# Kernel tuning notes

Hardware: AMD Instinct MI355X
Metric: run time of the kernel (lower is better)

## Reference

```python
import jax, jax.numpy as jnp
import numpy as np

N_NODES = 100000
N_EDGES = 3200000
N_FEAT = 512
N_CLASS = 10
HIDDEN = 16
EPS = 1e-12  # matches torch F.normalize clamp


def setup_inputs() -> dict:
    key = jax.random.key(0)
    ks = jax.random.split(key, 6)
    x = jax.random.normal(ks[0], (N_NODES, N_FEAT), dtype=jnp.float32)
    edge_index = jax.random.randint(ks[1], (2, N_EDGES), 0, N_NODES, dtype=jnp.int64)
    W1 = jax.random.normal(ks[2], (N_FEAT, HIDDEN), dtype=jnp.float32) / np.sqrt(N_FEAT)
    b1 = jnp.zeros((HIDDEN,), dtype=jnp.float32)
    beta = jnp.ones((1,), dtype=jnp.float32)  # learnable scalar of prop2
    W2 = jax.random.normal(ks[3], (HIDDEN, N_CLASS), dtype=jnp.float32) / np.sqrt(HIDDEN)
    b2 = jnp.zeros((N_CLASS,), dtype=jnp.float32)
    return {"x": x, "edge_index": edge_index, "W1": W1, "b1": b1,
            "beta": beta, "W2": W2, "b2": b2}


def _agnn_conv(h, src, dst, beta_val, n_nodes):
    # L2-normalize node features (cosine attention)
    norm = jnp.maximum(jnp.linalg.norm(h, axis=-1, keepdims=True), EPS)
    hn = h / norm
    # per-edge attention logit: beta * cos(h_i, h_j)
    alpha = beta_val * jnp.sum(hn[src] * hn[dst], axis=-1)  # [E]
    # scatter-softmax over edges sharing the same destination node
    amax = jax.ops.segment_max(alpha, dst, num_segments=n_nodes)
    ea = jnp.exp(alpha - amax[dst])
    denom = jax.ops.segment_sum(ea, dst, num_segments=n_nodes)
    w = ea / denom[dst]  # self-loops guarantee denom > 0
    # weighted aggregation of source features into destination nodes
    return jax.ops.segment_sum(w[:, None] * h[src], dst, num_segments=n_nodes)


def reference(x, edge_index, W1, b1, beta, W2, b2):
    n = x.shape[0]
    # dropout is identity in eval mode
    h = jax.nn.relu(x @ W1 + b1)  # [N, 16]
    # AGNNConv adds self-loops before propagation
    loops = jnp.arange(n, dtype=edge_index.dtype)
    src = jnp.concatenate([edge_index[0], loops])
    dst = jnp.concatenate([edge_index[1], loops])
    h = _agnn_conv(h, src, dst, jnp.float32(1.0), n)   # prop1: beta fixed to 1
    h = _agnn_conv(h, src, dst, beta[0], n)            # prop2: learnable beta
    logits = h @ W2 + b2
    return jax.nn.log_softmax(logits, axis=-1)
```

## Files before the change

kernel.cpp:

```cpp
#include <hip/hip_runtime.h>
#include <hip/hip_fp16.h>
#include <math.h>

#define N_NODES 100000
#define N_EDGES 3200000
#define EPRIME  (N_EDGES + N_NODES)
#define NFEAT   512
#define HID     16
#define NCLS    10

#define NPB     256
#define NB      ((N_NODES + NPB - 1) / NPB)
#define CHUNK   4096
#define NCH     ((EPRIME + CHUNK - 1) / CHUNK)
#define CAPB    10240
#define GBLK    2048

union U2 { unsigned int u; __half2 h; };
__device__ __forceinline__ float2 u2f(unsigned int v) {
  U2 t; t.u = v; return __half22float2(t.h);
}

__global__ __launch_bounds__(256, 4) void k_gemm_norm(const float* __restrict__ x,
                                                      const float* __restrict__ W1,
                                                      const float* __restrict__ b1,
                                                      __half* __restrict__ hn1,
                                                      float* __restrict__ norms1,
                                                      int* __restrict__ gcur) {
  if (blockIdx.x == 0)
    for (int i = threadIdx.x; i < NB; i += 256) gcur[i] = 0;

  __shared__ float red[2][2][2][16];

  const int lane = threadIdx.x & 63;
  const int wv   = threadIdx.x >> 6;
  const int r    = wv >> 1;
  const int h    = wv & 1;
  const int stride = GBLK * 2;
  const int row0 = blockIdx.x * 2 + r;
  const int nIter = (N_NODES - 1 - blockIdx.x * 2) / stride + 1;

  float4 w[4][4];
#pragma unroll
  for (int kk = 0; kk < 4; ++kk)
#pragma unroll
    for (int j = 0; j < 4; ++j)
      w[kk][j] = *reinterpret_cast<const float4*>(
          W1 + (size_t)(h * 256 + lane * 4 + kk) * 16 + j * 4);

  const float bias = (lane < 16) ? b1[lane] : 0.f;
  const int koff = h * 256 + lane * 4;

  const float4 z4 = make_float4(0.f, 0.f, 0.f, 0.f);
  float4 c0 = z4, p0 = z4, t0 = z4;

  if (row0 < N_NODES)
    c0 = *reinterpret_cast<const float4*>(x + (size_t)row0 * NFEAT + koff);
  if (row0 + stride < N_NODES)
    p0 = *reinterpret_cast<const float4*>(x + (size_t)(row0 + stride) * NFEAT + koff);

  for (int i = 0; i < nIter; ++i) {
    const int row = row0 + i * stride;
    const int r2 = row + 2 * stride;
    if (r2 < N_NODES)
      t0 = *reinterpret_cast<const float4*>(x + (size_t)r2 * NFEAT + koff);

    const float xs[4] = {c0.x, c0.y, c0.z, c0.w};

    float acc[16];
#pragma unroll
    for (int j = 0; j < 16; ++j) acc[j] = 0.f;

#pragma unroll
    for (int kk = 0; kk < 4; ++kk) {
      const float xv = xs[kk];
#pragma unroll
      for (int j4 = 0; j4 < 4; ++j4) {
        acc[j4 * 4 + 0] = fmaf(xv, w[kk][j4].x, acc[j4 * 4 + 0]);
        acc[j4 * 4 + 1] = fmaf(xv, w[kk][j4].y, acc[j4 * 4 + 1]);
        acc[j4 * 4 + 2] = fmaf(xv, w[kk][j4].z, acc[j4 * 4 + 2]);
        acc[j4 * 4 + 3] = fmaf(xv, w[kk][j4].w, acc[j4 * 4 + 3]);
      }
    }

#pragma unroll
    for (int j = 0; j < 8; ++j) {
      float send = (lane & 32) ? acc[j] : acc[j + 8];
      float rr = __shfl_xor(send, 32);
      acc[j] = ((lane & 32) ? acc[j + 8] : acc[j]) + rr;
    }
#pragma unroll
    for (int j = 0; j < 4; ++j) {
      float send = (lane & 16) ? acc[j] : acc[j + 4];
      float rr = __shfl_xor(send, 16);
      acc[j] = ((lane & 16) ? acc[j + 4] : acc[j]) + rr;
    }
#pragma unroll
    for (int j = 0; j < 2; ++j) {
      float send = (lane & 8) ? acc[j] : acc[j + 2];
      float rr = __shfl_xor(send, 8);
      acc[j] = ((lane & 8) ? acc[j + 2] : acc[j]) + rr;
    }
    {
      float send = (lane & 4) ? acc[0] : acc[1];
      float rr = __shfl_xor(send, 4);
      acc[0] = ((lane & 4) ? acc[1] : acc[0]) + rr;
    }
    acc[0] += __shfl_xor(acc[0], 2);
    acc[0] += __shfl_xor(acc[0], 1);

    if ((lane & 3) == 0) red[i & 1][r][h][lane >> 2] = acc[0];
    __syncthreads();

    if (h == 0 && row < N_NODES) {
      float v = 0.f;
      if (lane < 16)
        v = fmaxf(red[i & 1][r][0][lane] + red[i & 1][r][1][lane] + bias, 0.f);
      float ss = v * v;
      ss += __shfl_xor(ss, 1);
      ss += __shfl_xor(ss, 2);
      ss += __shfl_xor(ss, 4);
      ss += __shfl_xor(ss, 8);
      const float nrm = sqrtf(ss);
      const float inv = 1.0f / fmaxf(nrm, 1e-12f);
      if (lane < 16) hn1[(size_t)row * HID + lane] = __float2half_rn(v * inv);
      if (lane == 0) norms1[row] = nrm;
    }

    c0 = p0; p0 = t0;
  }
}

__global__ __launch_bounds__(256) void k_part(const int* __restrict__ ei,
                                              int* __restrict__ gcur,
                                              unsigned int* __restrict__ slots) {
  __shared__ int sh_hist[NB];
  __shared__ int sh_gbase[NB];
  const int tid = threadIdx.x;

  for (int i = tid; i < NB; i += 256) sh_hist[i] = 0;
  __syncthreads();

  const int base = blockIdx.x * CHUNK;
  unsigned int pk[16];
  int bk[16], rk[16];
#pragma unroll
  for (int j = 0; j < 16; ++j) {
    int e = base + j * 256 + tid;
    bool valid = (e < EPRIME);
    int srcv = 0, d = 0;
    if (valid) {
      if (e < N_EDGES) { srcv = ei[e]; d = ei[N_EDGES + e]; }
      else             { srcv = d = e - N_EDGES; }
    }
    bk[j] = valid ? (d >> 8) : -1;
    pk[j] = (unsigned)srcv | ((unsigned)(d & 255) << 20);
    rk[j] = valid ? atomicAdd(&sh_hist[d >> 8], 1) : 0;
  }
  __syncthreads();

  for (int i = tid; i < NB; i += 256) {
    int hc = sh_hist[i];
    sh_gbase[i] = hc ? atomicAdd(&gcur[i], hc) : 0;
  }
  __syncthreads();

#pragma unroll
  for (int j = 0; j < 16; ++j)
    if (bk[j] >= 0)
      slots[(size_t)bk[j] * CAPB + sh_gbase[bk[j]] + rk[j]] = pk[j];
}

__global__ __launch_bounds__(256) void k_csr(const unsigned int* __restrict__ slots,
                                             const int* __restrict__ gcur,
                                             unsigned int* __restrict__ csr,
                                             unsigned int* __restrict__ soffs,
                                             unsigned short* __restrict__ ecnt) {
  __shared__ int sh_cnt[NPB];
  __shared__ int sh_cnt2[NPB];
  __shared__ int sh_sc[NPB];
  __shared__ int sh_loffs[NPB];
  const int b = blockIdx.x, tid = threadIdx.x;
  const int ne = gcur[b];
  const unsigned int* my = slots + (size_t)b * CAPB;

  sh_cnt[tid] = 0;
  sh_cnt2[tid] = 0;
  __syncthreads();

  for (int i = tid; i < ne; i += 256) atomicAdd(&sh_cnt[my[i] >> 20], 1);
  __syncthreads();

  const int v = sh_cnt[tid];
  sh_sc[tid] = v;
  __syncthreads();
  for (int d = 1; d < NPB; d <<= 1) {
    int u = (tid >= d) ? sh_sc[tid - d] : 0;
    __syncthreads();
    sh_sc[tid] += u;
    __syncthreads();
  }
  const int excl = sh_sc[tid] - v;
  sh_loffs[tid] = excl;

  if (tid < 16) csr[(size_t)b * CAPB + ne + tid] = 0;

  const int node = b * NPB + tid;
  if (node < N_NODES) {
    soffs[node] = (unsigned)(b * CAPB + excl);
    ecnt[node]  = (unsigned short)v;
  }
  __syncthreads();

  for (int i = tid; i < ne; i += 256) {
    const unsigned pv = my[i];
    const int local = pv >> 20;
    const int rr = atomicAdd(&sh_cnt2[local], 1);
    csr[(size_t)b * CAPB + sh_loffs[local] + rr] = pv & 0xFFFFF;
  }
}

template <bool FINAL>
__device__ __forceinline__ void pull_body(const __half* __restrict__ hn,
                                          const float* __restrict__ norms,
                                          const unsigned int* __restrict__ soffs,
                                          const unsigned short* __restrict__ ecnt,
                                          const unsigned int* __restrict__ csr,
                                          float beta,
                                          __half* __restrict__ out_hn,
                                          float* __restrict__ out_norms,
                                          const float* __restrict__ W2,
                                          const float* __restrict__ b2,
                                          float* __restrict__ out) {
  const int node = blockIdx.x * 4 + (threadIdx.x >> 6);
  if (node >= N_NODES) return;
  const int lane = threadIdx.x & 63;
  const int q    = lane & 3;
  const int slot = lane >> 2;

  float w4x = 0.f, w4y = 0.f, w4z = 0.f, w4w = 0.f, b2v = 0.f;
  if (FINAL) {
    const int sc = (slot < NCLS) ? slot : 0;
    w4x = W2[(q * 4 + 0) * NCLS + sc];
    w4y = W2[(q * 4 + 1) * NCLS + sc];
    w4z = W2[(q * 4 + 2) * NCLS + sc];
    w4w = W2[(q * 4 + 3) * NCLS + sc];
    b2v = b2[sc];
  }

  const uint2 qraw = *reinterpret_cast<const uint2*>(hn + (size_t)node * HID + q * 4);
  const float2 qa = u2f(qraw.x), qb = u2f(qraw.y);
  const unsigned s = soffs[node];
  const unsigned e = s + ecnt[node];

  float den = 0.f;
  float ax = 0.f, ay = 0.f, az = 0.f, aw = 0.f;

  for (unsigned bi = s; bi < e; bi += 16) {
    const unsigned i = bi + slot;
    const int src = (int)csr[i];
    const uint2 rr = *reinterpret_cast<const uint2*>(hn + (size_t)src * HID + q * 4);
    const float2 f0 = u2f(rr.x), f1 = u2f(rr.y);
    float pd = qa.x * f0.x + qa.y * f0.y + qb.x * f1.x + qb.y * f1.y;
    pd += __shfl_xor(pd, 1);
    pd += __shfl_xor(pd, 2);
    const float t = (i < e) ? __expf(beta * pd) : 0.f;
    den += t;
    const float wgt = t * norms[src];
    ax += wgt * f0.x; ay += wgt * f0.y; az += wgt * f1.x; aw += wgt * f1.y;
  }

#pragma unroll
  for (int m = 4; m <= 32; m <<= 1) {
    den += __shfl_xor(den, m);
    ax  += __shfl_xor(ax, m);
    ay  += __shfl_xor(ay, m);
    az  += __shfl_xor(az, m);
    aw  += __shfl_xor(aw, m);
  }
  const float inv = 1.0f / den;
  ax *= inv; ay *= inv; az *= inv; aw *= inv;

  if (!FINAL) {
    float ssn = ax * ax + ay * ay + az * az + aw * aw;
    ssn += __shfl_xor(ssn, 1);
    ssn += __shfl_xor(ssn, 2);
    const float nrm = sqrtf(ssn);
    const float ninv = 1.0f / fmaxf(nrm, 1e-12f);
    if (lane < 4) {
      U2 lo, hi;
      lo.h = __floats2half2_rn(ax * ninv, ay * ninv);
      hi.h = __floats2half2_rn(az * ninv, aw * ninv);
      *reinterpret_cast<uint2*>(out_hn + (size_t)node * HID + q * 4) =
          make_uint2(lo.u, hi.u);
      if (lane == 0) out_norms[node] = nrm;
    }
  } else {
    float part = ax * w4x + ay * w4y + az * w4z + aw * w4w;
    part += __shfl_xor(part, 1);
    part += __shfl_xor(part, 2);
    const float logit = part + b2v;

    float lg[NCLS];
#pragma unroll
    for (int c = 0; c < NCLS; ++c) lg[c] = __shfl(logit, c * 4);
    float m = lg[0];
#pragma unroll
    for (int c = 1; c < NCLS; ++c) m = fmaxf(m, lg[c]);
    float se = 0.f;
#pragma unroll
    for (int c = 0; c < NCLS; ++c) se += __expf(lg[c] - m);
    const float ls = m + logf(se);

    const float myv = __shfl(logit, lane * 4);
    if (lane < NCLS) out[(size_t)node * NCLS + lane] = myv - ls;
  }
}

__global__ __launch_bounds__(256) void k_pull1(const __half* __restrict__ hn1,
                                               const float* __restrict__ norms1,
                                               const unsigned int* __restrict__ soffs,
                                               const unsigned short* __restrict__ ecnt,
                                               const unsigned int* __restrict__ csr,
                                               __half* __restrict__ hn2,
                                               float* __restrict__ norms2) {
  pull_body<false>(hn1, norms1, soffs, ecnt, csr, 1.0f, hn2, norms2,
                   nullptr, nullptr, nullptr);
}

__global__ __launch_bounds__(256) void k_pull2(const __half* __restrict__ hn2,
                                               const float* __restrict__ norms2,
                                               const unsigned int* __restrict__ soffs,
                                               const unsigned short* __restrict__ ecnt,
                                               const unsigned int* __restrict__ csr,
                                               const float* __restrict__ beta_ptr,
                                               const float* __restrict__ W2,
                                               const float* __restrict__ b2,
                                               float* __restrict__ out) {
  pull_body<true>(hn2, norms2, soffs, ecnt, csr, beta_ptr[0], nullptr, nullptr,
                  W2, b2, out);
}

extern "C" void kernel_launch(void* const* d_in, const int* in_sizes, int n_in,
                              void* d_out, int out_size, void* d_ws, size_t ws_size,
                              hipStream_t stream) {
  const float* x    = (const float*)d_in[0];
  const int*   ei   = (const int*)d_in[1];
  const float* W1   = (const float*)d_in[2];
  const float* b1   = (const float*)d_in[3];
  const float* beta = (const float*)d_in[4];
  const float* W2   = (const float*)d_in[5];
  const float* b2   = (const float*)d_in[6];
  float* out = (float*)d_out;

  char* p = (char*)d_ws;
  __half* hn1 = (__half*)p;                 p += (size_t)N_NODES * HID * 2;
  float* norms1 = (float*)p;                p += (size_t)N_NODES * 4;
  __half* hn2 = (__half*)p;                 p += (size_t)N_NODES * HID * 2;
  float* norms2 = (float*)p;                p += (size_t)N_NODES * 4;
  unsigned int* soffs = (unsigned int*)p;   p += (size_t)N_NODES * 4;
  unsigned short* ecnt = (unsigned short*)p; p += (size_t)N_NODES * 2 + 64;
  int* gcur = (int*)p;                      p += (size_t)NB * 4 + 32;
  unsigned int* csr = (unsigned int*)p;     p += ((size_t)NB * CAPB + 16) * 4;
  unsigned int* slots = (unsigned int*)p;

  k_gemm_norm<<<GBLK, 256, 0, stream>>>(x, W1, b1, hn1, norms1, gcur);
  k_part<<<NCH, 256, 0, stream>>>(ei, gcur, slots);
  k_csr<<<NB, 256, 0, stream>>>(slots, gcur, csr, soffs, ecnt);

  const int nblW = (N_NODES + 3) / 4;
  k_pull1<<<nblW, 256, 0, stream>>>(hn1, norms1, soffs, ecnt, csr, hn2, norms2);
  k_pull2<<<nblW, 256, 0, stream>>>(hn2, norms2, soffs, ecnt, csr, beta, W2, b2, out);
}
```

Before: 260.0 us.

## Compute first-layer GEMM with fp16 MFMA per 16-row wave tile

```diff
diff --git a/kernel.cpp b/kernel.cpp
--- a/kernel.cpp
+++ b/kernel.cpp
@@ -14,120 +14,83 @@
 #define CHUNK   4096
 #define NCH     ((EPRIME + CHUNK - 1) / CHUNK)
 #define CAPB    10240
-#define GBLK    2048
+#define NWAVE_G 6250
+#define GBLK    ((NWAVE_G + 3) / 4)
+
+typedef _Float16 f16x8 __attribute__((ext_vector_type(8)));
+typedef float f32x4 __attribute__((ext_vector_type(4)));
 
 union U2 { unsigned int u; __half2 h; };
 __device__ __forceinline__ float2 u2f(unsigned int v) {
   U2 t; t.u = v; return __half22float2(t.h);
 }
 
-__global__ __launch_bounds__(256, 4) void k_gemm_norm(const float* __restrict__ x,
-                                                      const float* __restrict__ W1,
-                                                      const float* __restrict__ b1,
-                                                      __half* __restrict__ hn1,
-                                                      float* __restrict__ norms1,
-                                                      int* __restrict__ gcur) {
+__global__ __launch_bounds__(256) void k_gemm_norm(const float* __restrict__ x,
+                                                   const float* __restrict__ W1,
+                                                   const float* __restrict__ b1,
+                                                   __half* __restrict__ hn1,
+                                                   float* __restrict__ norms1,
+                                                   int* __restrict__ gcur) {
   if (blockIdx.x == 0)
     for (int i = threadIdx.x; i < NB; i += 256) gcur[i] = 0;
 
-  __shared__ float red[2][2][2][16];
-
+  const int w = blockIdx.x * 4 + (threadIdx.x >> 6);
+  if (w >= NWAVE_G) return;
   const int lane = threadIdx.x & 63;
-  const int wv   = threadIdx.x >> 6;
-  const int r    = wv >> 1;
-  const int h    = wv & 1;
-  const int stride = GBLK * 2;
-  const int row0 = blockIdx.x * 2 + r;
-  const int nIter = (N_NODES - 1 - blockIdx.x * 2) / stride + 1;
-
-  float4 w[4][4];
-#pragma unroll
-  for (int kk = 0; kk < 4; ++kk)
-#pragma unroll
-    for (int j = 0; j < 4; ++j)
-      w[kk][j] = *reinterpret_cast<const float4*>(
-          W1 + (size_t)(h * 256 + lane * 4 + kk) * 16 + j * 4);
-
-  const float bias = (lane < 16) ? b1[lane] : 0.f;
-  const int koff = h * 256 + lane * 4;
-
-  const float4 z4 = make_float4(0.f, 0.f, 0.f, 0.f);
-  float4 c0 = z4, p0 = z4, t0 = z4;
-
-  if (row0 < N_NODES)
-    c0 = *reinterpret_cast<const float4*>(x + (size_t)row0 * NFEAT + koff);
-  if (row0 + stride < N_NODES)
-    p0 = *reinterpret_cast<const float4*>(x + (size_t)(row0 + stride) * NFEAT + koff);
-
-  for (int i = 0; i < nIter; ++i) {
-    const int row = row0 + i * stride;
-    const int r2 = row + 2 * stride;
-    if (r2 < N_NODES)
-      t0 = *reinterpret_cast<const float4*>(x + (size_t)r2 * NFEAT + koff);
-
-    const float xs[4] = {c0.x, c0.y, c0.z, c0.w};
-
-    float acc[16];
-#pragma unroll
-    for (int j = 0; j < 16; ++j) acc[j] = 0.f;
-
-#pragma unroll
-    for (int kk = 0; kk < 4; ++kk) {
-      const float xv = xs[kk];
-#pragma unroll
-      for (int j4 = 0; j4 < 4; ++j4) {
-        acc[j4 * 4 + 0] = fmaf(xv, w[kk][j4].x, acc[j4 * 4 + 0]);
-        acc[j4 * 4 + 1] = fmaf(xv, w[kk][j4].y, acc[j4 * 4 + 1]);
-        acc[j4 * 4 + 2] = fmaf(xv, w[kk][j4].z, acc[j4 * 4 + 2]);
-        acc[j4 * 4 + 3] = fmaf(xv, w[kk][j4].w, acc[j4 * 4 + 3]);
-      }
+  const int col  = lane & 15;
+  const int g    = lane >> 4;
+  const int r0   = w * 16;
+
+  f16x8 bf[16];
+#pragma unroll
+  for (int t = 0; t < 16; ++t)
+#pragma unroll
+    for (int j = 0; j < 8; ++j)
+      bf[t][j] = (_Float16)W1[(t * 32 + g * 8 + j) * 16 + col];
+
+  const float* xr = x + (size_t)(r0 + col) * NFEAT + g * 8;
+
+  f32x4 acc = {0.f, 0.f, 0.f, 0.f};
+  float4 a0 = *reinterpret_cast<const float4*>(xr);
+  float4 a1 = *reinterpret_cast<const float4*>(xr + 4);
+
+#pragma unroll
+  for (int t = 0; t < 16; ++t) {
+    float4 n0, n1;
+    if (t < 15) {
+      n0 = *reinterpret_cast<const float4*>(xr + (t + 1) * 32);
+      n1 = *reinterpret_cast<const float4*>(xr + (t + 1) * 32 + 4);
     }
-
-#pragma unroll
-    for (int j = 0; j < 8; ++j) {
-      float send = (lane & 32) ? acc[j] : acc[j + 8];
-      float rr = __shfl_xor(send, 32);
-      acc[j] = ((lane & 32) ? acc[j + 8] : acc[j]) + rr;
-    }
-#pragma unroll
-    for (int j = 0; j < 4; ++j) {
-      float send = (lane & 16) ? acc[j] : acc[j + 4];
-      float rr = __shfl_xor(send, 16);
-      acc[j] = ((lane & 16) ? acc[j + 4] : acc[j]) + rr;
-    }
-#pragma unroll
-    for (int j = 0; j < 2; ++j) {
-      float send = (lane & 8) ? acc[j] : acc[j + 2];
-      float rr = __shfl_xor(send, 8);
-      acc[j] = ((lane & 8) ? acc[j + 2] : acc[j]) + rr;
-    }
-    {
-      float send = (lane & 4) ? acc[0] : acc[1];
-      float rr = __shfl_xor(send, 4);
-      acc[0] = ((lane & 4) ? acc[1] : acc[0]) + rr;
-    }
-    acc[0] += __shfl_xor(acc[0], 2);
-    acc[0] += __shfl_xor(acc[0], 1);
-
-    if ((lane & 3) == 0) red[i & 1][r][h][lane >> 2] = acc[0];
-    __syncthreads();
-
-    if (h == 0 && row < N_NODES) {
-      float v = 0.f;
-      if (lane < 16)
-        v = fmaxf(red[i & 1][r][0][lane] + red[i & 1][r][1][lane] + bias, 0.f);
-      float ss = v * v;
-      ss += __shfl_xor(ss, 1);
-      ss += __shfl_xor(ss, 2);
-      ss += __shfl_xor(ss, 4);
-      ss += __shfl_xor(ss, 8);
-      const float nrm = sqrtf(ss);
-      const float inv = 1.0f / fmaxf(nrm, 1e-12f);
-      if (lane < 16) hn1[(size_t)row * HID + lane] = __float2half_rn(v * inv);
-      if (lane == 0) norms1[row] = nrm;
-    }
-
-    c0 = p0; p0 = t0;
+    f16x8 af;
+    af[0] = (_Float16)a0.x; af[1] = (_Float16)a0.y;
+    af[2] = (_Float16)a0.z; af[3] = (_Float16)a0.w;
+    af[4] = (_Float16)a1.x; af[5] = (_Float16)a1.y;
+    af[6] = (_Float16)a1.z; af[7] = (_Float16)a1.w;
+    acc = __builtin_amdgcn_mfma_f32_16x16x32_f16(af, bf[t], acc, 0, 0, 0);
+    if (t < 15) { a0 = n0; a1 = n1; }
+  }
+
+  const float bias = b1[col];
+  float v[4], ss[4];
+#pragma unroll
+  for (int c = 0; c < 4; ++c) {
+    v[c] = fmaxf(acc[c] + bias, 0.f);
+    ss[c] = v[c] * v[c];
+  }
+#pragma unroll
+  for (int c = 0; c < 4; ++c) {
+    ss[c] += __shfl_xor(ss[c], 1);
+    ss[c] += __shfl_xor(ss[c], 2);
+    ss[c] += __shfl_xor(ss[c], 4);
+    ss[c] += __shfl_xor(ss[c], 8);
+  }
+#pragma unroll
+  for (int c = 0; c < 4; ++c) {
+    const int r = r0 + g * 4 + c;
+    const float nrm = sqrtf(ss[c]);
+    const float inv = 1.0f / fmaxf(nrm, 1e-12f);
+    hn1[(size_t)r * HID + col] = __float2half_rn(v[c] * inv);
+    if (col == c) norms1[r] = nrm;
   }
 }
 
```

Result: faster. 223.3 us (-14.1%).
